# Performance work log

Hardware: AMD Instinct MI355X
Metric: run time of the kernel (lower is better)

The kernel has to match this reference:

```python
import jax, jax.numpy as jnp
import numpy as np

NU = 3
NUM_MEM_TOKENS = 128
EPS = 1e-5


def dpfp(x, nu=NU):
    # x: [..., d] -> [..., 2*nu*d]; all outputs are >= 0
    x = jnp.concatenate([jax.nn.relu(x), jax.nn.relu(-x)], axis=-1)
    x_rolled = jnp.concatenate([jnp.roll(x, shift=j, axis=-1) for j in range(1, nu + 1)], axis=-1)
    x_repeat = jnp.concatenate([x] * nu, axis=-1)
    return x_repeat * x_rolled


def setup_inputs() -> dict:
    key = jax.random.key(0)
    ks = jax.random.split(key, 8)
    B, S, D, DM = 1, 16384, 2048, 64
    DK = 2 * NU * DM  # 384
    scale = 0.02
    return {
        "hidden_states": jax.random.normal(ks[0], (B, S, D), jnp.float32),
        "Wmq": jax.random.normal(ks[1], (DM, D), jnp.float32) * scale,
        "Wmk": jax.random.normal(ks[2], (DM, D), jnp.float32) * scale,
        "Wmv": jax.random.normal(ks[3], (D, D), jnp.float32) * scale,
        "Wmb_w": jax.random.normal(ks[4], (1, D), jnp.float32) * scale,
        "Wmb_b": jax.random.normal(ks[5], (1,), jnp.float32),
        "W_mem": jax.random.normal(ks[6], (B, DK, D), jnp.float32) * scale,
        "z": jax.random.uniform(ks[7], (B, DK), jnp.float32) + 0.1,
    }


def reference(hidden_states, Wmq, Wmk, Wmv, Wmb_w, Wmb_b, W_mem, z):
    # ---- associate (read from fast-weight memory) ----
    mq = dpfp(hidden_states @ Wmq.T)                       # [b,s,dk]
    num = jnp.einsum('ijk,ikt->ijt', mq, W_mem)            # [b,s,d]
    denom = jnp.einsum('ik,ijk->ij', z, mq)[..., None] + EPS
    hidden_states = num / denom + hidden_states

    # wrapped transformer layer modeled as identity
    out = hidden_states

    # ---- update_mem (write: recurrent outer-product accumulation) ----
    mem_tokens = out[:, -NUM_MEM_TOKENS:]                  # [b,m,d]
    mk = dpfp(mem_tokens @ Wmk.T)                          # [b,m,dk]
    new_mv = mem_tokens @ Wmv.T                            # [b,m,d]

    num2 = jnp.einsum('ijk,ikt->ijt', mk, W_mem)           # [b,m,d]
    denom2 = jnp.einsum('ij,ikj->ik', z, mk)[..., None] + EPS
    prev_mv = num2 / denom2

    mk_sq = jnp.sum(mk * mk, axis=-1)                      # ||mk||^2, [b,m]
    new_info_coef = 1.0 - denom2 / (mk_sq + EPS)[..., None]
    new_info_coef = jax.lax.stop_gradient(jnp.clip(new_info_coef, 0.0, 1.0))

    mv = new_mv - prev_mv
    mb = jax.nn.sigmoid(mem_tokens @ Wmb_w.T + Wmb_b)[..., 0]  # [b,m]
    associations = jnp.einsum('ijk,ijt,ij->ikt', mk, mv, mb)   # [b,dk,d]

    W_mem_new = W_mem + associations
    z_new = z + jnp.sum(new_info_coef * mk, axis=1)
    return out, W_mem_new, z_new
```

## Files before the change

kernel.cpp:

```cpp
#include <hip/hip_runtime.h>
#include <hip/hip_bf16.h>
#include <math.h>

#define S_ 16384
#define D_ 2048
#define DM_ 64
#define DK_ 384
#define NMEM_ 128
#define EPS_ 1e-5f

typedef __attribute__((ext_vector_type(8))) short bf16x8;
typedef __attribute__((ext_vector_type(8))) short s16x8;
typedef __attribute__((ext_vector_type(4))) float f32x4;
typedef unsigned short u16;

static __device__ __forceinline__ u16 f2bf(float x) {
    __hip_bfloat16 h = __float2bfloat16(x);
    return *reinterpret_cast<u16*>(&h);
}

static __device__ __forceinline__ float bf2f(u16 u) {
    union { unsigned int i; float f; } c; c.i = ((unsigned int)u) << 16;
    return c.f;
}

static __device__ __forceinline__ void gload16(const void* g, void* l) {
    __builtin_amdgcn_global_load_lds(
        (const __attribute__((address_space(1))) unsigned int*)g,
        (__attribute__((address_space(3))) unsigned int*)l, 16, 0, 0);
}

__global__ __launch_bounds__(256) void k_prep(const float* __restrict__ Wmq,
                                              const float* __restrict__ Wmv,
                                              const float* __restrict__ Wmem,
                                              u16* __restrict__ Wmq_b,
                                              u16* __restrict__ Wmv_b,
                                              u16* __restrict__ WmT) {
    __shared__ float ts[32][33];
    const int bid = blockIdx.x;
    const int tid = threadIdx.x;
    if (bid < 4096) {
        size_t idx = ((size_t)bid * 256 + tid) * 4;
        float4 v = *reinterpret_cast<const float4*>(&Wmv[idx]);
        ushort4 p;
        p.x = f2bf(v.x); p.y = f2bf(v.y); p.z = f2bf(v.z); p.w = f2bf(v.w);
        *reinterpret_cast<ushort4*>(&Wmv_b[idx]) = p;
    } else if (bid < 4224) {
        int idx = ((bid - 4096) * 256 + tid) * 4;
        float4 v = *reinterpret_cast<const float4*>(&Wmq[idx]);
        ushort4 p;
        p.x = f2bf(v.x); p.y = f2bf(v.y); p.z = f2bf(v.z); p.w = f2bf(v.w);
        *reinterpret_cast<ushort4*>(&Wmq_b[idx]) = p;
    } else {
        int t = bid - 4224;
        int c0 = (t & 63) * 32, k0 = (t >> 6) * 32;
        const int tx = tid & 31, ty = tid >> 5;
#pragma unroll
        for (int i = 0; i < 4; ++i)
            ts[ty + 8 * i][tx] = Wmem[(size_t)(k0 + ty + 8 * i) * D_ + c0 + tx];
        __syncthreads();
#pragma unroll
        for (int i = 0; i < 4; ++i)
            WmT[(size_t)(c0 + ty + 8 * i) * DK_ + k0 + tx] = f2bf(ts[tx][ty + 8 * i]);
    }
}

__global__ __launch_bounds__(256) void k_fuse(const float* __restrict__ hs,
                                              const u16* __restrict__ Wmq_b,
                                              const u16* __restrict__ WmT,
                                              const float* __restrict__ z,
                                              float* __restrict__ out) {
    __shared__ u16 sbuf[16384];
    __shared__ float zs[DK_];
    __shared__ float dinvS[32];
    const int r0 = blockIdx.x * 32;
    const int tid = threadIdx.x;
    const int lane = tid & 63, w = tid >> 6;
    const int lrow = lane & 15, lkg = lane >> 4;
    const int wr = w >> 1, wc = w & 1;
    for (int i = tid; i < DK_; i += 256) zs[i] = z[i];

    u16* As = sbuf;
    u16* Bs = sbuf + 2048;
    f32x4 q1[2];
    const f32x4 zero4 = {0.f, 0.f, 0.f, 0.f};
    q1[0] = zero4; q1[1] = zero4;
    for (int kc = 0; kc < D_ / 64; ++kc) {
#pragma unroll
        for (int i = 0; i < 2; ++i) {
            int flat4 = tid + 256 * i;
            int row = flat4 >> 4, c4 = flat4 & 15;
            const float4 v = *reinterpret_cast<const float4*>(
                &hs[(size_t)(r0 + row) * D_ + kc * 64 + c4 * 4]);
            int off = row * 64 + (((c4 >> 1) ^ (row & 7)) * 8) + (c4 & 1) * 4;
            ushort4 p;
            p.x = f2bf(v.x); p.y = f2bf(v.y); p.z = f2bf(v.z); p.w = f2bf(v.w);
            *reinterpret_cast<ushort4*>(&As[off]) = p;
        }
#pragma unroll
        for (int i = 0; i < 2; ++i) {
            int col = w * 16 + i * 8 + (lane >> 3);
            int gg = (lane & 7) ^ (col & 7);
            gload16(Wmq_b + (size_t)col * D_ + kc * 64 + gg * 8,
                    &Bs[(w * 16 + i * 8) * 64]);
        }
        __syncthreads();
#pragma unroll
        for (int s = 0; s < 2; ++s) {
            int rl = wr * 16 + lrow;
            bf16x8 a_ = *reinterpret_cast<const bf16x8*>(
                &As[rl * 64 + (((s * 4 + lkg) ^ (rl & 7)) * 8)]);
#pragma unroll
            for (int n = 0; n < 2; ++n) {
                int cl = wc * 32 + n * 16 + lrow;
                bf16x8 b_ = *reinterpret_cast<const bf16x8*>(
                    &Bs[cl * 64 + (((s * 4 + lkg) ^ (cl & 7)) * 8)]);
                q1[n] = __builtin_amdgcn_mfma_f32_16x16x32_bf16(a_, b_, q1[n], 0, 0, 0);
            }
        }
        __syncthreads();
    }

    u16* xs = sbuf;
#pragma unroll
    for (int n = 0; n < 2; ++n) {
        int col = wc * 32 + n * 16 + lrow;
#pragma unroll
        for (int r = 0; r < 4; ++r) {
            int row = wr * 16 + lkg * 4 + r;
            float qv = q1[n][r];
            xs[row * 136 + col] = f2bf(fmaxf(qv, 0.f));
            xs[row * 136 + col + 64] = f2bf(fmaxf(-qv, 0.f));
        }
    }
    __syncthreads();

    bf16x8 af[12];
    float pd = 0.f;
    {
        int arow = wr * 16 + lrow;
#pragma unroll
        for (int f = 0; f < 12; ++f) {
            bf16x8 pk;
#pragma unroll
            for (int e = 0; e < 8; ++e) {
                int m = f * 32 + lkg * 8 + e;
                int g = m >> 7, i = m & 127;
                float v = bf2f(xs[arow * 136 + i]) *
                          bf2f(xs[arow * 136 + ((i - g - 1) & 127)]);
                pd += zs[m] * v;
                pk[e] = (short)f2bf(v);
            }
            af[f] = pk;
        }
        pd += __shfl_xor(pd, 16);
        pd += __shfl_xor(pd, 32);
        if (wc == 0 && lane < 16) dinvS[wr * 16 + lane] = 1.f / (pd + EPS_);
    }
    __syncthreads();

    f32x4 acc[4];
#pragma unroll
    for (int n = 0; n < 4; ++n) acc[n] = zero4;
    for (int ct = 0; ct < 16; ++ct) {
        const int c0 = ct * 128;
        for (int kc = 0; kc < 3; ++kc) {
#pragma unroll
            for (int i = 0; i < 8; ++i) {
                int flat = w * 64 + (lane) + 256 * i;
                int cc = flat >> 4, g4 = flat & 15;
                int gswz = g4 ^ (cc & 7);
                gload16(WmT + (size_t)(c0 + cc) * DK_ + kc * 128 + gswz * 8,
                        &sbuf[(w * 64 + 256 * i) * 8]);
            }
            __syncthreads();
#pragma unroll
            for (int s = 0; s < 4; ++s) {
#pragma unroll
                for (int n = 0; n < 4; ++n) {
                    int cl = wc * 64 + n * 16 + lrow;
                    bf16x8 bb = *reinterpret_cast<const bf16x8*>(
                        &sbuf[cl * 128 + (((s * 4 + lkg) ^ (cl & 7)) * 8)]);
                    acc[n] = __builtin_amdgcn_mfma_f32_16x16x32_bf16(
                        af[kc * 4 + s], bb, acc[n], 0, 0, 0);
                }
            }
            __syncthreads();
        }
#pragma unroll
        for (int n = 0; n < 4; ++n) {
            int colg = c0 + wc * 64 + n * 16 + lrow;
#pragma unroll
            for (int r = 0; r < 4; ++r) {
                int rowl = wr * 16 + lkg * 4 + r;
                size_t off = (size_t)(r0 + rowl) * D_ + colg;
                out[off] = acc[n][r] * dinvS[rowl] + hs[off];
            }
            acc[n] = zero4;
        }
    }
}

__global__ __launch_bounds__(256) void k_mk(const float* __restrict__ out,
                                            const float* __restrict__ Wmk,
                                            const float* __restrict__ Wmb_w,
                                            const float* __restrict__ Wmb_b,
                                            const float* __restrict__ z,
                                            float* __restrict__ mk_g,
                                            u16* __restrict__ mk_b,
                                            u16* __restrict__ mem_b,
                                            float* __restrict__ scal) {
    __shared__ float memRow[D_];
    __shared__ float qpart[4][64];
    __shared__ float xv[128];
    __shared__ float mks[DK_];
    __shared__ float red[256];
    const int j = blockIdx.x;
    const int tid = threadIdx.x;
    const float* mem = out + (size_t)(S_ - NMEM_ + j) * D_;
    const float4* mem4 = reinterpret_cast<const float4*>(mem);
    float4* mr4 = reinterpret_cast<float4*>(memRow);
#pragma unroll
    for (int i4 = tid; i4 < 512; i4 += 256) {
        float4 v = mem4[i4];
        mr4[i4] = v;
        ushort4 p;
        p.x = f2bf(v.x); p.y = f2bf(v.y); p.z = f2bf(v.z); p.w = f2bf(v.w);
        *reinterpret_cast<ushort4*>(&mem_b[(size_t)j * D_ + i4 * 4]) = p;
    }
    __syncthreads();
    {
        int c = tid & 63, seg = tid >> 6;
        const float4* wrow = reinterpret_cast<const float4*>(Wmk + (size_t)c * D_);
        float p = 0.f;
#pragma unroll 4
        for (int k4 = seg * 128; k4 < seg * 128 + 128; ++k4) {
            float4 a = mr4[k4], b = wrow[k4];
            p += a.x * b.x + a.y * b.y + a.z * b.z + a.w * b.w;
        }
        qpart[seg][c] = p;
    }
    __syncthreads();
    if (tid < 64) {
        float q = qpart[0][tid] + qpart[1][tid] + qpart[2][tid] + qpart[3][tid];
        xv[tid] = fmaxf(q, 0.f);
        xv[tid + 64] = fmaxf(-q, 0.f);
    }
    __syncthreads();
    for (int m = tid; m < DK_; m += 256) {
        int i = m & 127, g = m >> 7;
        float v = xv[i] * xv[(i - g - 1) & 127];
        mks[m] = v;
        mk_g[(size_t)j * DK_ + m] = v;
        mk_b[(size_t)j * DK_ + m] = f2bf(v);
    }
    __syncthreads();
    float pd = 0.f, ps = 0.f;
    for (int m = tid; m < DK_; m += 256) { float v = mks[m]; pd += v * z[m]; ps += v * v; }
    red[tid] = pd; __syncthreads();
    for (int s = 128; s > 0; s >>= 1) { if (tid < s) red[tid] += red[tid + s]; __syncthreads(); }
    float denom2 = red[0] + EPS_;
    __syncthreads();
    red[tid] = ps; __syncthreads();
    for (int s = 128; s > 0; s >>= 1) { if (tid < s) red[tid] += red[tid + s]; __syncthreads(); }
    float mksq = red[0];
    __syncthreads();
    float pb = 0.f;
    {
        const float4* wb4 = reinterpret_cast<const float4*>(Wmb_w);
#pragma unroll
        for (int k4 = tid; k4 < 512; k4 += 256) {
            float4 a = mr4[k4], b = wb4[k4];
            pb += a.x * b.x + a.y * b.y + a.z * b.z + a.w * b.w;
        }
    }
    red[tid] = pb; __syncthreads();
    for (int s = 128; s > 0; s >>= 1) { if (tid < s) red[tid] += red[tid + s]; __syncthreads(); }
    if (tid == 0) {
        float bsum = red[0] + Wmb_b[0];
        float mb = 1.f / (1.f + expf(-bsum));
        float nic = 1.f - denom2 / (mksq + EPS_);
        nic = fminf(fmaxf(nic, 0.f), 1.f);
        scal[j * 4 + 0] = denom2;
        scal[j * 4 + 1] = nic;
        scal[j * 4 + 2] = mb;
        scal[j * 4 + 3] = mksq;
    }
}

__global__ __launch_bounds__(256) void k_mv(const u16* __restrict__ mem_b,
                                            const u16* __restrict__ Wmv_b,
                                            const u16* __restrict__ mk_b,
                                            const u16* __restrict__ WmT,
                                            const float* __restrict__ scal,
                                            float* __restrict__ mvb) {
    __shared__ u16 At[128 * 64];
    __shared__ u16 Bt[64 * 64];
    __shared__ float inv2[128];
    __shared__ float mbl[128];
    const int c0 = blockIdx.x * 64;
    const int tid = threadIdx.x;
    const int lane = tid & 63, w = tid >> 6;
    const int lrow = lane & 15, lkg = lane >> 4;
    const int wr = w >> 1, wc = w & 1;
    if (tid < 128) {
        inv2[tid] = 1.f / scal[tid * 4 + 0];
        mbl[tid] = scal[tid * 4 + 2];
    }
    f32x4 acc1[4][2], acc2[4][2];
    const f32x4 zero4 = {0.f, 0.f, 0.f, 0.f};
#pragma unroll
    for (int m = 0; m < 4; ++m)
#pragma unroll
        for (int n = 0; n < 2; ++n) { acc1[m][n] = zero4; acc2[m][n] = zero4; }
    for (int kc = 0; kc < D_ / 64; ++kc) {
#pragma unroll
        for (int i = 0; i < 4; ++i) {
            int rr = w * 32 + i * 8 + (lane >> 3);
            int gg = (lane & 7) ^ (rr & 7);
            gload16(mem_b + (size_t)rr * D_ + kc * 64 + gg * 8,
                    &At[(w * 32 + i * 8) * 64]);
        }
#pragma unroll
        for (int i = 0; i < 2; ++i) {
            int cc = w * 16 + i * 8 + (lane >> 3);
            int gg = (lane & 7) ^ (cc & 7);
            gload16(Wmv_b + (size_t)(c0 + cc) * D_ + kc * 64 + gg * 8,
                    &Bt[(w * 16 + i * 8) * 64]);
        }
        __syncthreads();
#pragma unroll
        for (int s = 0; s < 2; ++s) {
            bf16x8 af[4], bb[2];
#pragma unroll
            for (int m = 0; m < 4; ++m) {
                int rl = wr * 64 + m * 16 + lrow;
                af[m] = *reinterpret_cast<const bf16x8*>(
                    &At[rl * 64 + (((s * 4 + lkg) ^ (rl & 7)) * 8)]);
            }
#pragma unroll
            for (int n = 0; n < 2; ++n) {
                int cl = wc * 32 + n * 16 + lrow;
                bb[n] = *reinterpret_cast<const bf16x8*>(
                    &Bt[cl * 64 + (((s * 4 + lkg) ^ (cl & 7)) * 8)]);
            }
#pragma unroll
            for (int m = 0; m < 4; ++m)
#pragma unroll
                for (int n = 0; n < 2; ++n)
                    acc1[m][n] = __builtin_amdgcn_mfma_f32_16x16x32_bf16(
                        af[m], bb[n], acc1[m][n], 0, 0, 0);
        }
        __syncthreads();
    }
    for (int kc = 0; kc < 6; ++kc) {
#pragma unroll
        for (int i = 0; i < 4; ++i) {
            int rr = w * 32 + i * 8 + (lane >> 3);
            int gg = (lane & 7) ^ (rr & 7);
            gload16(mk_b + (size_t)rr * DK_ + kc * 64 + gg * 8,
                    &At[(w * 32 + i * 8) * 64]);
        }
#pragma unroll
        for (int i = 0; i < 2; ++i) {
            int cc = w * 16 + i * 8 + (lane >> 3);
            int gg = (lane & 7) ^ (cc & 7);
            gload16(WmT + (size_t)(c0 + cc) * DK_ + kc * 64 + gg * 8,
                    &Bt[(w * 16 + i * 8) * 64]);
        }
        __syncthreads();
#pragma unroll
        for (int s = 0; s < 2; ++s) {
            bf16x8 af[4], bb[2];
#pragma unroll
            for (int m = 0; m < 4; ++m) {
                int rl = wr * 64 + m * 16 + lrow;
                af[m] = *reinterpret_cast<const bf16x8*>(
                    &At[rl * 64 + (((s * 4 + lkg) ^ (rl & 7)) * 8)]);
            }
#pragma unroll
            for (int n = 0; n < 2; ++n) {
                int cl = wc * 32 + n * 16 + lrow;
                bb[n] = *reinterpret_cast<const bf16x8*>(
                    &Bt[cl * 64 + (((s * 4 + lkg) ^ (cl & 7)) * 8)]);
            }
#pragma unroll
            for (int m = 0; m < 4; ++m)
#pragma unroll
                for (int n = 0; n < 2; ++n)
                    acc2[m][n] = __builtin_amdgcn_mfma_f32_16x16x32_bf16(
                        af[m], bb[n], acc2[m][n], 0, 0, 0);
        }
        __syncthreads();
    }
#pragma unroll
    for (int m = 0; m < 4; ++m)
#pragma unroll
        for (int n = 0; n < 2; ++n) {
            int colg = c0 + wc * 32 + n * 16 + lrow;
#pragma unroll
            for (int r = 0; r < 4; ++r) {
                int j = wr * 64 + m * 16 + lkg * 4 + r;
                mvb[(size_t)j * D_ + colg] =
                    (acc1[m][n][r] - acc2[m][n][r] * inv2[j]) * mbl[j];
            }
        }
}

__global__ __launch_bounds__(256) void k_wmem(const float* __restrict__ Wmem,
                                              const float* __restrict__ mk_g,
                                              const float* __restrict__ mvb,
                                              const float* __restrict__ scal,
                                              const float* __restrict__ z,
                                              float* __restrict__ wout,
                                              float* __restrict__ zout) {
    const int tid = threadIdx.x;
    if (blockIdx.y == 48) {
        if (blockIdx.x == 0) {
            for (int t = tid; t < DK_; t += 256) {
                float acc = z[t];
                for (int j = 0; j < NMEM_; ++j)
                    acc += scal[j * 4 + 1] * mk_g[(size_t)j * DK_ + t];
                zout[t] = acc;
            }
        }
        return;
    }
    const int c0 = blockIdx.x * 256;
    const int k0 = blockIdx.y * 8;
    const int tk = tid >> 5, tt = tid & 31;
    const float4* mvb4 = reinterpret_cast<const float4*>(mvb);
    f32x4 acc[2] = {{0.f, 0.f, 0.f, 0.f}, {0.f, 0.f, 0.f, 0.f}};
#pragma unroll 4
    for (int j = 0; j < NMEM_; ++j) {
        float a = mk_g[(size_t)j * DK_ + k0 + tk];
#pragma unroll
        for (int i = 0; i < 2; ++i) {
            float4 v = mvb4[((size_t)j * D_ + c0 + tt * 4 + 128 * i) >> 2];
            acc[i][0] += a * v.x; acc[i][1] += a * v.y;
            acc[i][2] += a * v.z; acc[i][3] += a * v.w;
        }
    }
#pragma unroll
    for (int i = 0; i < 2; ++i) {
        size_t off = (size_t)(k0 + tk) * D_ + c0 + tt * 4 + 128 * i;
        float4 wv = *reinterpret_cast<const float4*>(&Wmem[off]);
        float4 o;
        o.x = wv.x + acc[i][0]; o.y = wv.y + acc[i][1];
        o.z = wv.z + acc[i][2]; o.w = wv.w + acc[i][3];
        *reinterpret_cast<float4*>(&wout[off]) = o;
    }
}

extern "C" void kernel_launch(void* const* d_in, const int* in_sizes, int n_in,
                              void* d_out, int out_size, void* d_ws, size_t ws_size,
                              hipStream_t stream) {
    const float* hs   = (const float*)d_in[0];
    const float* Wmq  = (const float*)d_in[1];
    const float* Wmk  = (const float*)d_in[2];
    const float* Wmv  = (const float*)d_in[3];
    const float* Wmbw = (const float*)d_in[4];
    const float* Wmbb = (const float*)d_in[5];
    const float* Wmem = (const float*)d_in[6];
    const float* z    = (const float*)d_in[7];
    float* out  = (float*)d_out;
    float* wout = out + (size_t)S_ * D_;
    float* zout = wout + (size_t)DK_ * D_;

    float* ws = (float*)d_ws;
    float* mk_g   = ws;
    float* scal   = mk_g + (size_t)NMEM_ * DK_;
    float* mvb    = scal + NMEM_ * 4;
    u16* WmT   = (u16*)(mvb + (size_t)NMEM_ * D_);
    u16* Wmq_b = WmT + (size_t)D_ * DK_;
    u16* Wmv_b = Wmq_b + (size_t)DM_ * D_;
    u16* mem_b = Wmv_b + (size_t)D_ * D_;
    u16* mk_b  = mem_b + (size_t)NMEM_ * D_;

    k_prep<<<dim3(4992), 256, 0, stream>>>(Wmq, Wmv, Wmem, Wmq_b, Wmv_b, WmT);
    k_fuse<<<dim3(S_ / 32), 256, 0, stream>>>(hs, Wmq_b, WmT, z, out);
    k_mk<<<dim3(NMEM_), 256, 0, stream>>>(out, Wmk, Wmbw, Wmbb, z, mk_g, mk_b, mem_b, scal);
    k_mv<<<dim3(D_ / 64), 256, 0, stream>>>(mem_b, Wmv_b, mk_b, WmT, scal, mvb);
    k_wmem<<<dim3(D_ / 256, DK_ / 8 + 1), 256, 0, stream>>>(Wmem, mk_g, mvb, scal, z, wout, zout);
}
```

Baseline: 236.2 us.

## Enlarge fused read kernel to 64-row tiles with double-buffered WmT pipeline

```diff
diff --git a/kernel.cpp b/kernel.cpp
--- a/kernel.cpp
+++ b/kernel.cpp
@@ -65,30 +65,30 @@
     }
 }
 
-__global__ __launch_bounds__(256) void k_fuse(const float* __restrict__ hs,
-                                              const u16* __restrict__ Wmq_b,
-                                              const u16* __restrict__ WmT,
-                                              const float* __restrict__ z,
-                                              float* __restrict__ out) {
-    __shared__ u16 sbuf[16384];
+__global__ __launch_bounds__(512) void k_fuseA(const float* __restrict__ hs,
+                                               const u16* __restrict__ Wmq_b,
+                                               const u16* __restrict__ WmT,
+                                               const float* __restrict__ z,
+                                               float* __restrict__ out) {
+    __shared__ u16 mqs[64 * 384];
+    __shared__ u16 scratch[16384];
     __shared__ float zs[DK_];
-    __shared__ float dinvS[32];
-    const int r0 = blockIdx.x * 32;
+    __shared__ float dinvS[64];
+    const int r0 = blockIdx.x * 64;
     const int tid = threadIdx.x;
     const int lane = tid & 63, w = tid >> 6;
     const int lrow = lane & 15, lkg = lane >> 4;
-    const int wr = w >> 1, wc = w & 1;
-    for (int i = tid; i < DK_; i += 256) zs[i] = z[i];
-
-    u16* As = sbuf;
-    u16* Bs = sbuf + 2048;
-    f32x4 q1[2];
     const f32x4 zero4 = {0.f, 0.f, 0.f, 0.f};
-    q1[0] = zero4; q1[1] = zero4;
+
+    u16* As = scratch;
+    u16* Bs = scratch + 4096;
+    const int wrp = w >> 2, wcp = w & 3;
+    f32x4 q[2];
+    q[0] = zero4; q[1] = zero4;
     for (int kc = 0; kc < D_ / 64; ++kc) {
 #pragma unroll
         for (int i = 0; i < 2; ++i) {
-            int flat4 = tid + 256 * i;
+            int flat4 = tid + 512 * i;
             int row = flat4 >> 4, c4 = flat4 & 15;
             const float4 v = *reinterpret_cast<const float4*>(
                 &hs[(size_t)(r0 + row) * D_ + kc * 64 + c4 * 4]);
@@ -97,107 +97,143 @@
             p.x = f2bf(v.x); p.y = f2bf(v.y); p.z = f2bf(v.z); p.w = f2bf(v.w);
             *reinterpret_cast<ushort4*>(&As[off]) = p;
         }
-#pragma unroll
-        for (int i = 0; i < 2; ++i) {
-            int col = w * 16 + i * 8 + (lane >> 3);
-            int gg = (lane & 7) ^ (col & 7);
-            gload16(Wmq_b + (size_t)col * D_ + kc * 64 + gg * 8,
-                    &Bs[(w * 16 + i * 8) * 64]);
-        }
+        gload16(Wmq_b + (size_t)(w * 8 + (lane >> 3)) * D_ + kc * 64
+                      + ((lane & 7) ^ (lane >> 3)) * 8,
+                Bs + w * 512);
         __syncthreads();
 #pragma unroll
         for (int s = 0; s < 2; ++s) {
-            int rl = wr * 16 + lrow;
-            bf16x8 a_ = *reinterpret_cast<const bf16x8*>(
-                &As[rl * 64 + (((s * 4 + lkg) ^ (rl & 7)) * 8)]);
-#pragma unroll
-            for (int n = 0; n < 2; ++n) {
-                int cl = wc * 32 + n * 16 + lrow;
-                bf16x8 b_ = *reinterpret_cast<const bf16x8*>(
-                    &Bs[cl * 64 + (((s * 4 + lkg) ^ (cl & 7)) * 8)]);
-                q1[n] = __builtin_amdgcn_mfma_f32_16x16x32_bf16(a_, b_, q1[n], 0, 0, 0);
-            }
-        }
-        __syncthreads();
-    }
-
-    u16* xs = sbuf;
-#pragma unroll
-    for (int n = 0; n < 2; ++n) {
-        int col = wc * 32 + n * 16 + lrow;
-#pragma unroll
-        for (int r = 0; r < 4; ++r) {
-            int row = wr * 16 + lkg * 4 + r;
-            float qv = q1[n][r];
-            xs[row * 136 + col] = f2bf(fmaxf(qv, 0.f));
-            xs[row * 136 + col + 64] = f2bf(fmaxf(-qv, 0.f));
-        }
-    }
-    __syncthreads();
-
-    bf16x8 af[12];
-    float pd = 0.f;
+            bf16x8 af[2];
+#pragma unroll
+            for (int m = 0; m < 2; ++m) {
+                int rl = wrp * 32 + m * 16 + lrow;
+                af[m] = *reinterpret_cast<const bf16x8*>(
+                    &As[rl * 64 + (((s * 4 + lkg) ^ (rl & 7)) * 8)]);
+            }
+            int cl = wcp * 16 + lrow;
+            bf16x8 b_ = *reinterpret_cast<const bf16x8*>(
+                &Bs[cl * 64 + (((s * 4 + lkg) ^ (cl & 7)) * 8)]);
+            q[0] = __builtin_amdgcn_mfma_f32_16x16x32_bf16(af[0], b_, q[0], 0, 0, 0);
+            q[1] = __builtin_amdgcn_mfma_f32_16x16x32_bf16(af[1], b_, q[1], 0, 0, 0);
+        }
+        __syncthreads();
+    }
+
+    u16* xs = scratch;
     {
-        int arow = wr * 16 + lrow;
-#pragma unroll
-        for (int f = 0; f < 12; ++f) {
-            bf16x8 pk;
+        int col = wcp * 16 + lrow;
+#pragma unroll
+        for (int m = 0; m < 2; ++m)
+#pragma unroll
+            for (int r = 0; r < 4; ++r) {
+                int row = wrp * 32 + m * 16 + lkg * 4 + r;
+                float qv = q[m][r];
+                xs[row * 136 + col] = f2bf(fmaxf(qv, 0.f));
+                xs[row * 136 + col + 64] = f2bf(fmaxf(-qv, 0.f));
+            }
+    }
+    if (tid < DK_) zs[tid] = z[tid];
+    __syncthreads();
+    {
+        int row = tid >> 3, sub = tid & 7;
+        float pd = 0.f;
+#pragma unroll
+        for (int c = 0; c < 6; ++c) {
+            int base = sub * 48 + c * 8;
+            int g = base >> 7;
+            int gm = base >> 3;
+            s16x8 pk;
 #pragma unroll
             for (int e = 0; e < 8; ++e) {
-                int m = f * 32 + lkg * 8 + e;
-                int g = m >> 7, i = m & 127;
-                float v = bf2f(xs[arow * 136 + i]) *
-                          bf2f(xs[arow * 136 + ((i - g - 1) & 127)]);
+                int m = base + e;
+                int i = m & 127;
+                float v = bf2f(xs[row * 136 + i]) *
+                          bf2f(xs[row * 136 + ((i - g - 1) & 127)]);
                 pd += zs[m] * v;
                 pk[e] = (short)f2bf(v);
             }
-            af[f] = pk;
-        }
-        pd += __shfl_xor(pd, 16);
-        pd += __shfl_xor(pd, 32);
-        if (wc == 0 && lane < 16) dinvS[wr * 16 + lane] = 1.f / (pd + EPS_);
-    }
-    __syncthreads();
-
-    f32x4 acc[4];
-#pragma unroll
-    for (int n = 0; n < 4; ++n) acc[n] = zero4;
-    for (int ct = 0; ct < 16; ++ct) {
-        const int c0 = ct * 128;
-        for (int kc = 0; kc < 3; ++kc) {
-#pragma unroll
-            for (int i = 0; i < 8; ++i) {
-                int flat = w * 64 + (lane) + 256 * i;
-                int cc = flat >> 4, g4 = flat & 15;
-                int gswz = g4 ^ (cc & 7);
-                gload16(WmT + (size_t)(c0 + cc) * DK_ + kc * 128 + gswz * 8,
-                        &sbuf[(w * 64 + 256 * i) * 8]);
-            }
-            __syncthreads();
-#pragma unroll
-            for (int s = 0; s < 4; ++s) {
-#pragma unroll
-                for (int n = 0; n < 4; ++n) {
-                    int cl = wc * 64 + n * 16 + lrow;
-                    bf16x8 bb = *reinterpret_cast<const bf16x8*>(
-                        &sbuf[cl * 128 + (((s * 4 + lkg) ^ (cl & 7)) * 8)]);
-                    acc[n] = __builtin_amdgcn_mfma_f32_16x16x32_bf16(
-                        af[kc * 4 + s], bb, acc[n], 0, 0, 0);
+            int slot = gm ^ (row & 7);
+            *reinterpret_cast<s16x8*>(&mqs[row * 384 + slot * 8]) = pk;
+        }
+        pd += __shfl_down(pd, 4, 8);
+        pd += __shfl_down(pd, 2, 8);
+        pd += __shfl_down(pd, 1, 8);
+        if (sub == 0) dinvS[row] = 1.f / (pd + EPS_);
+    }
+    __syncthreads();
+
+    u16* Bs0 = scratch;
+    u16* Bs1 = scratch + 8192;
+    const int wr3 = w >> 2, wc3 = w & 3;
+    f32x4 acc[2][2];
+#pragma unroll
+    for (int m = 0; m < 2; ++m)
+#pragma unroll
+        for (int n = 0; n < 2; ++n) acc[m][n] = zero4;
+#pragma unroll
+    for (int i = 0; i < 2; ++i) {
+        int j = w * 2 + i;
+        int rowc = j * 8 + (lane >> 3);
+        gload16(WmT + (size_t)rowc * DK_ + ((lane & 7) ^ (rowc & 7)) * 8,
+                Bs0 + j * 512);
+    }
+    __syncthreads();
+    int cur = 0;
+    for (int rr = 0; rr < 96; ++rr) {
+        const int ct = rr / 6, kc = rr % 6;
+        if (rr + 1 < 96) {
+            const int ct2 = (rr + 1) / 6, kc2 = (rr + 1) % 6;
+            u16* bnext = cur ? Bs0 : Bs1;
+#pragma unroll
+            for (int i = 0; i < 2; ++i) {
+                int j = w * 2 + i;
+                int rowc = j * 8 + (lane >> 3);
+                gload16(WmT + (size_t)(ct2 * 128 + rowc) * DK_ + kc2 * 64
+                              + ((lane & 7) ^ (rowc & 7)) * 8,
+                        bnext + j * 512);
+            }
+        }
+        u16* bcur = cur ? Bs1 : Bs0;
+#pragma unroll
+        for (int s = 0; s < 2; ++s) {
+            bf16x8 af[2], bb[2];
+#pragma unroll
+            for (int m = 0; m < 2; ++m) {
+                int rl = wr3 * 32 + m * 16 + lrow;
+                int G = kc * 8 + s * 4 + lkg;
+                af[m] = *reinterpret_cast<const bf16x8*>(
+                    &mqs[rl * 384 + ((G ^ (rl & 7)) * 8)]);
+            }
+#pragma unroll
+            for (int n = 0; n < 2; ++n) {
+                int cl = wc3 * 32 + n * 16 + lrow;
+                bb[n] = *reinterpret_cast<const bf16x8*>(
+                    &bcur[cl * 64 + (((s * 4 + lkg) ^ (cl & 7)) * 8)]);
+            }
+#pragma unroll
+            for (int m = 0; m < 2; ++m)
+#pragma unroll
+                for (int n = 0; n < 2; ++n)
+                    acc[m][n] = __builtin_amdgcn_mfma_f32_16x16x32_bf16(
+                        af[m], bb[n], acc[m][n], 0, 0, 0);
+        }
+        if (kc == 5) {
+#pragma unroll
+            for (int m = 0; m < 2; ++m)
+#pragma unroll
+                for (int n = 0; n < 2; ++n) {
+                    int colg = ct * 128 + wc3 * 32 + n * 16 + lrow;
+#pragma unroll
+                    for (int r4 = 0; r4 < 4; ++r4) {
+                        int rowl = wr3 * 32 + m * 16 + lkg * 4 + r4;
+                        size_t off = (size_t)(r0 + rowl) * D_ + colg;
+                        out[off] = acc[m][n][r4] * dinvS[rowl] + hs[off];
+                    }
+                    acc[m][n] = zero4;
                 }
-            }
-            __syncthreads();
-        }
-#pragma unroll
-        for (int n = 0; n < 4; ++n) {
-            int colg = c0 + wc * 64 + n * 16 + lrow;
-#pragma unroll
-            for (int r = 0; r < 4; ++r) {
-                int rowl = wr * 16 + lkg * 4 + r;
-                size_t off = (size_t)(r0 + rowl) * D_ + colg;
-                out[off] = acc[n][r] * dinvS[rowl] + hs[off];
-            }
-            acc[n] = zero4;
-        }
+        }
+        __syncthreads();
+        cur ^= 1;
     }
 }
 
@@ -478,7 +514,7 @@
     u16* mk_b  = mem_b + (size_t)NMEM_ * D_;
 
     k_prep<<<dim3(4992), 256, 0, stream>>>(Wmq, Wmv, Wmem, Wmq_b, Wmv_b, WmT);
-    k_fuse<<<dim3(S_ / 32), 256, 0, stream>>>(hs, Wmq_b, WmT, z, out);
+    k_fuseA<<<dim3(S_ / 64), 512, 0, stream>>>(hs, Wmq_b, WmT, z, out);
     k_mk<<<dim3(NMEM_), 256, 0, stream>>>(out, Wmk, Wmbw, Wmbb, z, mk_g, mk_b, mem_b, scal);
     k_mv<<<dim3(D_ / 64), 256, 0, stream>>>(mem_b, Wmv_b, mk_b, WmT, scal, mvb);
     k_wmem<<<dim3(D_ / 256, DK_ / 8 + 1), 256, 0, stream>>>(Wmem, mk_g, mvb, scal, z, wout, zout);
```

Result: faster. 203.8 us (-13.7%).
